# Optimization experiments

Hardware: AMD Instinct MI355X
Metric: run time of the kernel (lower is better)

## Reference

```python
import jax, jax.numpy as jnp
import numpy as np
import math

D = 1024
H = 16
DH = D // H
B, M, N = 4, 1024, 2048
LN_EPS = 1e-5


def setup_inputs() -> dict:
    key = jax.random.key(0)
    ks = jax.random.split(key, 8)
    s = 1.0 / math.sqrt(D)  # keep logits well-scaled
    return {
        "Q": jax.random.normal(ks[0], (B, M, D), jnp.float32),
        "KV": jax.random.normal(ks[1], (B, N, D), jnp.float32),
        "log_gate_bias": jax.random.normal(ks[2], (B, N), jnp.float32),
        "Wq": jax.random.normal(ks[3], (D, D), jnp.float32) * s,
        "bq": jnp.zeros((D,), jnp.float32),
        "Wk": jax.random.normal(ks[4], (D, D), jnp.float32) * s,
        "bk": jnp.zeros((D,), jnp.float32),
        "Wv": jax.random.normal(ks[5], (D, D), jnp.float32) * s,
        "bv": jnp.zeros((D,), jnp.float32),
        "Wo": jax.random.normal(ks[6], (D, D), jnp.float32) * s,
        "bo": jnp.zeros((D,), jnp.float32),
        "gamma": jnp.ones((D,), jnp.float32),
        "beta": jnp.zeros((D,), jnp.float32),
    }


def reference(Q, KV, log_gate_bias, Wq, bq, Wk, bk, Wv, bv, Wo, bo, gamma, beta):
    b, m, d = Q.shape
    n = KV.shape[1]
    # projections (torch Linear: x @ W.T + b), split heads -> (b, h, len, dh)
    q = (Q @ Wq.T + bq).reshape(b, m, H, DH).transpose(0, 2, 1, 3)
    k = (KV @ Wk.T + bk).reshape(b, n, H, DH).transpose(0, 2, 1, 3)
    v = (KV @ Wv.T + bv).reshape(b, n, H, DH).transpose(0, 2, 1, 3)
    scores = jnp.einsum('bhmd,bhnd->bhmn', q, k) / math.sqrt(DH)
    # additive gate bias broadcast over heads and queries: (b,1,1,n)
    scores = scores + log_gate_bias[:, None, None, :]
    attn = jax.nn.softmax(scores, axis=-1)
    out = jnp.einsum('bhmn,bhnd->bhmd', attn, v)
    out = out.transpose(0, 2, 1, 3).reshape(b, m, d)
    out = out @ Wo.T + bo
    # dropout p=0.0 (eval) -> identity; residual + LayerNorm
    x = Q + out
    mu = jnp.mean(x, axis=-1, keepdims=True)
    var = jnp.mean(jnp.square(x - mu), axis=-1, keepdims=True)
    return gamma * (x - mu) * jax.lax.rsqrt(var + LN_EPS) + beta
```

## Files before the change

kernel.cpp:

```cpp
#include <hip/hip_runtime.h>
#include <hip/hip_bf16.h>

#define DMODEL 1024
#define NHEAD  16
#define DHEAD  64
#define BB     4
#define MM     1024
#define NN     2048
#define LOG2E  1.4426950408889634f

typedef __attribute__((ext_vector_type(8))) short bf16x8;
typedef __attribute__((ext_vector_type(4))) float f32x4;

#define AS1 __attribute__((address_space(1)))
#define AS3 __attribute__((address_space(3)))

__device__ __forceinline__ unsigned short f2bf(float f) {
  unsigned int u = __builtin_bit_cast(unsigned int, f);
  unsigned int r = (u + 0x7fffu + ((u >> 16) & 1u)) >> 16;
  return (unsigned short)r;
}
__device__ __forceinline__ float bf2f(unsigned int u16) {
  return __builtin_bit_cast(float, u16 << 16);
}

__global__ __launch_bounds__(256)
void cast_all(const float* __restrict__ Q, const float* __restrict__ KV,
              const float* __restrict__ W0, const float* __restrict__ W1,
              const float* __restrict__ W2, const float* __restrict__ W3,
              unsigned short* __restrict__ oQ, unsigned short* __restrict__ oKV,
              unsigned short* __restrict__ o0, unsigned short* __restrict__ o1,
              unsigned short* __restrict__ o2, unsigned short* __restrict__ o3)
{
  const int bid = blockIdx.x;
  const float* s; unsigned short* d; int i;
  if (bid < 4096)       { s = Q;  d = oQ;  i = bid * 256 + threadIdx.x; }
  else if (bid < 12288) { s = KV; d = oKV; i = (bid - 4096) * 256 + threadIdx.x; }
  else {
    const int w = (bid - 12288) >> 10;
    s = w == 0 ? W0 : w == 1 ? W1 : w == 2 ? W2 : W3;
    d = w == 0 ? o0 : w == 1 ? o1 : w == 2 ? o2 : o3;
    i = ((bid - 12288) & 1023) * 256 + threadIdx.x;
  }
  const float4 v = ((const float4*)s)[i];
  union { unsigned short us[4]; unsigned long long u64; } o;
  o.us[0] = f2bf(v.x); o.us[1] = f2bf(v.y); o.us[2] = f2bf(v.z); o.us[3] = f2bf(v.w);
  *(unsigned long long*)(d + (size_t)i * 4) = o.u64;
}

__global__ __launch_bounds__(256)
void qkv_gemm(const unsigned short* __restrict__ Qbf,
              const unsigned short* __restrict__ KVbf,
              const unsigned short* __restrict__ Wqb,
              const unsigned short* __restrict__ Wkb,
              const unsigned short* __restrict__ Wvb,
              const float* __restrict__ bq, const float* __restrict__ bk,
              const float* __restrict__ bv,
              unsigned short* __restrict__ qout,
              unsigned short* __restrict__ kout,
              unsigned short* __restrict__ vtout)
{
  __shared__ unsigned short As[3][128 * 32];
  __shared__ unsigned short Ws[3][128 * 32];

  const int bid = blockIdx.x;
  const unsigned short* A; const unsigned short* W; const float* bias;
  int mode, lb, nmb;
  if (bid < 256)      { A = Qbf;  W = Wqb; bias = bq; mode = 0; lb = bid;       nmb = 4; }
  else if (bid < 768) { A = KVbf; W = Wkb; bias = bk; mode = 1; lb = bid - 256; nmb = 8; }
  else                { A = KVbf; W = Wvb; bias = bv; mode = 2; lb = bid - 768; nmb = 8; }
  const int xcd = lb & 7;
  const int l   = lb >> 3;
  const int mb  = xcd * nmb + (l >> 3);
  const int nb  = l & 7;

  const int tid  = threadIdx.x;
  const int wave = tid >> 6;
  const int lane = tid & 63;
  const int l15  = lane & 15;
  const int l4   = lane >> 4;
  const int wm   = wave >> 1;
  const int wn   = wave & 1;
  const size_t row0 = (size_t)mb * 128;
  const size_t col0 = (size_t)nb * 128;

  f32x4 acc[4][4] = {};

  const int cc0 = (wave * 2) * 64 + lane;
  const int cc1 = cc0 + 64;
  const int r0 = cc0 >> 2, sch0 = (cc0 & 3) ^ (r0 & 3);
  const int r1 = cc1 >> 2, sch1 = (cc1 & 3) ^ (r1 & 3);
  const unsigned short* ap0 = A + (row0 + r0) * DMODEL + sch0 * 8;
  const unsigned short* ap1 = A + (row0 + r1) * DMODEL + sch1 * 8;
  const unsigned short* wp0 = W + (col0 + r0) * DMODEL + sch0 * 8;
  const unsigned short* wp1 = W + (col0 + r1) * DMODEL + sch1 * 8;

  auto stage = [&](int buf) {
    __builtin_amdgcn_global_load_lds((const AS1 void*)ap0, (AS3 void*)(&As[buf][cc0 * 8]), 16, 0, 0);
    __builtin_amdgcn_global_load_lds((const AS1 void*)ap1, (AS3 void*)(&As[buf][cc1 * 8]), 16, 0, 0);
    __builtin_amdgcn_global_load_lds((const AS1 void*)wp0, (AS3 void*)(&Ws[buf][cc0 * 8]), 16, 0, 0);
    __builtin_amdgcn_global_load_lds((const AS1 void*)wp1, (AS3 void*)(&Ws[buf][cc1 * 8]), 16, 0, 0);
    ap0 += 32; ap1 += 32; wp0 += 32; wp1 += 32;
  };

  stage(0);
  stage(1);

  int cur = 0;
  for (int kt = 0; kt < 32; ++kt) {
    if (kt < 31) {
      asm volatile("s_waitcnt vmcnt(4)" ::: "memory");
    } else {
      asm volatile("s_waitcnt vmcnt(0)" ::: "memory");
    }
    __builtin_amdgcn_sched_barrier(0);
    __builtin_amdgcn_s_barrier();
    __builtin_amdgcn_sched_barrier(0);
    if (kt < 30) {
      int nxt = cur + 2; if (nxt >= 3) nxt -= 3;
      stage(nxt);
    }

    bf16x8 af[4], bfr[4];
#pragma unroll
    for (int mi = 0; mi < 4; ++mi) {
      int r = wm * 64 + mi * 16 + l15;
      af[mi] = *(const bf16x8*)&As[cur][r * 32 + ((l4 ^ (r & 3)) << 3)];
    }
#pragma unroll
    for (int ni = 0; ni < 4; ++ni) {
      int r = wn * 64 + ni * 16 + l15;
      bfr[ni] = *(const bf16x8*)&Ws[cur][r * 32 + ((l4 ^ (r & 3)) << 3)];
    }
    __builtin_amdgcn_s_setprio(1);
#pragma unroll
    for (int mi = 0; mi < 4; ++mi)
#pragma unroll
      for (int ni = 0; ni < 4; ++ni)
        acc[mi][ni] = __builtin_amdgcn_mfma_f32_16x16x32_bf16(af[mi], bfr[ni], acc[mi][ni], 0, 0, 0);
    __builtin_amdgcn_s_setprio(0);

    cur = (cur == 2) ? 0 : cur + 1;
  }

#pragma unroll
  for (int mi = 0; mi < 4; ++mi) {
#pragma unroll
    for (int ni = 0; ni < 4; ++ni) {
      const int col = (int)col0 + wn * 64 + ni * 16 + l15;
      const float bcol = bias[col];
      if (mode == 2) {
        const int row = (int)row0 + wm * 64 + mi * 16 + l4 * 4;
        const int b = row >> 11, n = row & 2047;
        const int h = col >> 6, d = col & 63;
        union { unsigned short us[4]; uint2 u; } pk;
#pragma unroll
        for (int i = 0; i < 4; ++i)
          pk.us[i] = __builtin_bit_cast(unsigned short, __float2bfloat16(acc[mi][ni][i] + bcol));
        *(uint2*)(vtout + (((size_t)(b * 16 + h) * 64 + d) << 11) + n) = pk.u;
      } else {
#pragma unroll
        for (int i = 0; i < 4; ++i) {
          const size_t row = row0 + wm * 64 + mi * 16 + l4 * 4 + i;
          float v = acc[mi][ni][i] + bcol;
          if (mode == 0) v *= (0.125f * LOG2E);
          (mode == 0 ? qout : kout)[row * DMODEL + col] =
            __builtin_bit_cast(unsigned short, __float2bfloat16(v));
        }
      }
    }
  }
}

__global__ __launch_bounds__(256)
void gemm_o(const unsigned short* __restrict__ A,
            const unsigned short* __restrict__ W,
            const float* __restrict__ bias,
            const unsigned short* __restrict__ resid,
            unsigned short* __restrict__ out)
{
  __shared__ unsigned short As[3][64 * 32];
  __shared__ unsigned short Ws[3][128 * 32];

  const int bid = blockIdx.x;
  const int xcd = bid & 7;
  const int l   = bid >> 3;
  const int mb  = xcd * 8 + (l >> 3);
  const int nb  = l & 7;

  const int tid  = threadIdx.x;
  const int wave = tid >> 6;
  const int lane = tid & 63;
  const int l15  = lane & 15;
  const int l4   = lane >> 4;
  const int wm   = wave >> 1;
  const int wn   = wave & 1;
  const size_t row0 = (size_t)mb * 64;
  const size_t col0 = (size_t)nb * 128;

  f32x4 acc[2][4] = {};

  const int ra = tid >> 2, scha = (tid & 3) ^ (ra & 3);
  const int cc0 = (wave * 2) * 64 + lane;
  const int cc1 = cc0 + 64;
  const int r0 = cc0 >> 2, sch0 = (cc0 & 3) ^ (r0 & 3);
  const int r1 = cc1 >> 2, sch1 = (cc1 & 3) ^ (r1 & 3);
  const unsigned short* ap  = A + (row0 + ra) * DMODEL + scha * 8;
  const unsigned short* wp0 = W + (col0 + r0) * DMODEL + sch0 * 8;
  const unsigned short* wp1 = W + (col0 + r1) * DMODEL + sch1 * 8;

  auto stage = [&](int buf) {
    __builtin_amdgcn_global_load_lds((const AS1 void*)ap,  (AS3 void*)(&As[buf][tid * 8]), 16, 0, 0);
    __builtin_amdgcn_global_load_lds((const AS1 void*)wp0, (AS3 void*)(&Ws[buf][cc0 * 8]), 16, 0, 0);
    __builtin_amdgcn_global_load_lds((const AS1 void*)wp1, (AS3 void*)(&Ws[buf][cc1 * 8]), 16, 0, 0);
    ap += 32; wp0 += 32; wp1 += 32;
  };

  stage(0);
  stage(1);

  int cur = 0;
  for (int kt = 0; kt < 32; ++kt) {
    if (kt < 31) {
      asm volatile("s_waitcnt vmcnt(3)" ::: "memory");
    } else {
      asm volatile("s_waitcnt vmcnt(0)" ::: "memory");
    }
    __builtin_amdgcn_sched_barrier(0);
    __builtin_amdgcn_s_barrier();
    __builtin_amdgcn_sched_barrier(0);
    if (kt < 30) {
      int nxt = cur + 2; if (nxt >= 3) nxt -= 3;
      stage(nxt);
    }

    bf16x8 af[2], bfr[4];
#pragma unroll
    for (int mi = 0; mi < 2; ++mi) {
      int r = wm * 32 + mi * 16 + l15;
      af[mi] = *(const bf16x8*)&As[cur][r * 32 + ((l4 ^ (r & 3)) << 3)];
    }
#pragma unroll
    for (int ni = 0; ni < 4; ++ni) {
      int r = wn * 64 + ni * 16 + l15;
      bfr[ni] = *(const bf16x8*)&Ws[cur][r * 32 + ((l4 ^ (r & 3)) << 3)];
    }
    __builtin_amdgcn_s_setprio(1);
#pragma unroll
    for (int mi = 0; mi < 2; ++mi)
#pragma unroll
      for (int ni = 0; ni < 4; ++ni)
        acc[mi][ni] = __builtin_amdgcn_mfma_f32_16x16x32_bf16(af[mi], bfr[ni], acc[mi][ni], 0, 0, 0);
    __builtin_amdgcn_s_setprio(0);

    cur = (cur == 2) ? 0 : cur + 1;
  }

#pragma unroll
  for (int mi = 0; mi < 2; ++mi) {
#pragma unroll
    for (int ni = 0; ni < 4; ++ni) {
      const int col = (int)col0 + wn * 64 + ni * 16 + l15;
      const float bcol = bias[col];
#pragma unroll
      for (int i = 0; i < 4; ++i) {
        const size_t row = row0 + wm * 32 + mi * 16 + l4 * 4 + i;
        const size_t idx = row * DMODEL + col;
        const float v = bf2f(resid[idx]) + acc[mi][ni][i] + bcol;
        out[idx] = __builtin_bit_cast(unsigned short, __float2bfloat16(v));
      }
    }
  }
}

__global__ __launch_bounds__(512, 4)
void attn_kernel(const unsigned short* __restrict__ qb,
                 const unsigned short* __restrict__ kb,
                 const unsigned short* __restrict__ vt,
                 const float* __restrict__ lgb,
                 unsigned short* __restrict__ attn)
{
  __shared__ unsigned short Ks[3][64 * 64];
  __shared__ unsigned short Vs[3][64 * 64];
  __shared__ float Gs[3][64];
  __shared__ unsigned short Ps[8][16 * 64];

  const int tid  = threadIdx.x;
  const int wave = tid >> 6;
  const int lane = tid & 63;
  const int l15  = lane & 15;
  const int l4   = lane >> 4;

  const int bid  = blockIdx.x;
  const int xcd  = bid & 7;
  const int slot = bid >> 3;
  const int m_i  = slot & 7;
  const int grp  = slot >> 3;
  const int bh   = grp * 8 + xcd;
  const int b    = bh >> 4;
  const int h    = bh & 15;
  const int m0   = m_i * 128;

  const unsigned short* qg = qb + ((size_t)(b * MM + m0)) * DMODEL + h * DHEAD;
  const unsigned short* kg = kb + ((size_t)b * NN) * DMODEL + h * DHEAD;
  const unsigned short* vg = vt + ((size_t)(b * NHEAD + h)) * (DHEAD * (size_t)NN);

  bf16x8 qf0, qf1;
  {
    const unsigned short* qrow = qg + (size_t)(wave * 16 + l15) * DMODEL;
    qf0 = *(const bf16x8*)(qrow + l4 * 8);
    qf1 = *(const bf16x8*)(qrow + 32 + l4 * 8);
  }

  bf16x8 ones;
  {
    const short one = (l15 == 0) ? (short)0x3f80 : (short)0;
#pragma unroll
    for (int j = 0; j < 8; ++j) ones[j] = one;
  }

  const int sr = tid >> 3;
  const int sc = (tid & 7) ^ (sr & 7);
  const unsigned short* kp = kg + (size_t)sr * DMODEL + (sc << 3);
  const unsigned short* vp = vg + (size_t)sr * NN + (sc << 3);
  const float* gp = lgb + (size_t)b * NN + lane;

  auto stage = [&](int buf) {
    if (wave == 0)
      __builtin_amdgcn_global_load_lds((const AS1 void*)gp, (AS3 void*)(&Gs[buf][lane]), 4, 0, 0);
    __builtin_amdgcn_global_load_lds((const AS1 void*)kp, (AS3 void*)(&Ks[buf][tid * 8]), 16, 0, 0);
    __builtin_amdgcn_global_load_lds((const AS1 void*)vp, (AS3 void*)(&Vs[buf][tid * 8]), 16, 0, 0);
    kp += 64 * DMODEL; vp += 64; gp += 64;
  };

  stage(0);
  stage(1);

  f32x4 ovec[5] = {};
  unsigned short* Pw = &Ps[wave][0];
  const int pbase = l15 * 128;
  const int s7 = l15 & 7;

  int cur = 0;
  for (int nt = 0; nt < NN / 64; ++nt) {
    if (nt < NN / 64 - 1) {
      if (wave == 0) asm volatile("s_waitcnt vmcnt(3)" ::: "memory");
      else           asm volatile("s_waitcnt vmcnt(2)" ::: "memory");
    } else {
      asm volatile("s_waitcnt vmcnt(0)" ::: "memory");
    }
    __builtin_amdgcn_sched_barrier(0);
    __builtin_amdgcn_s_barrier();
    __builtin_amdgcn_sched_barrier(0);
    if (nt < NN / 64 - 2) {
      int nxt = cur + 2; if (nxt >= 3) nxt -= 3;
      stage(nxt);
    }

    f32x4 s[4];
    __builtin_amdgcn_s_setprio(1);
#pragma unroll
    for (int ni = 0; ni < 4; ++ni) {
      const int r = ni * 16 + l15;
      const int c0 = l4 ^ (r & 7);
      bf16x8 kf0 = *(const bf16x8*)&Ks[cur][r * 64 + (c0 << 3)];
      bf16x8 kf1 = *(const bf16x8*)&Ks[cur][r * 64 + ((c0 ^ 4) << 3)];
      f32x4 z = {};
      z = __builtin_amdgcn_mfma_f32_16x16x32_bf16(kf0, qf0, z, 0, 0, 0);
      s[ni] = __builtin_amdgcn_mfma_f32_16x16x32_bf16(kf1, qf1, z, 0, 0, 0);
    }
    __builtin_amdgcn_s_setprio(0);

#pragma unroll
    for (int ni = 0; ni < 4; ++ni) {
      const float4 g = *(const float4*)&Gs[cur][ni * 16 + l4 * 4];
      union { unsigned short us[4]; uint2 u; } pk;
      pk.us[0] = __builtin_bit_cast(unsigned short,
                   __float2bfloat16(__builtin_amdgcn_exp2f(fmaf(g.x, LOG2E, s[ni][0]))));
      pk.us[1] = __builtin_bit_cast(unsigned short,
                   __float2bfloat16(__builtin_amdgcn_exp2f(fmaf(g.y, LOG2E, s[ni][1]))));
      pk.us[2] = __builtin_bit_cast(unsigned short,
                   __float2bfloat16(__builtin_amdgcn_exp2f(fmaf(g.z, LOG2E, s[ni][2]))));
      pk.us[3] = __builtin_bit_cast(unsigned short,
                   __float2bfloat16(__builtin_amdgcn_exp2f(fmaf(g.w, LOG2E, s[ni][3]))));
      *(uint2*)((char*)Pw + pbase + (((ni * 4 + l4) ^ (s7 << 1)) << 3)) = pk.u;
    }
    asm volatile("s_waitcnt lgkmcnt(0)" ::: "memory");
    __builtin_amdgcn_sched_barrier(0);

    __builtin_amdgcn_s_setprio(1);
#pragma unroll
    for (int ks2 = 0; ks2 < 2; ++ks2) {
      const bf16x8 pf = *(const bf16x8*)((const char*)Pw + pbase + (((ks2 * 4 + l4) ^ s7) << 4));
#pragma unroll
      for (int di = 0; di < 4; ++di) {
        const int d = di * 16 + l15;
        const bf16x8 vf = *(const bf16x8*)&Vs[cur][d * 64 + (((ks2 * 4 + l4) ^ (d & 7)) << 3)];
        ovec[di] = __builtin_amdgcn_mfma_f32_16x16x32_bf16(pf, vf, ovec[di], 0, 0, 0);
      }
      ovec[4] = __builtin_amdgcn_mfma_f32_16x16x32_bf16(pf, ones, ovec[4], 0, 0, 0);
    }
    __builtin_amdgcn_s_setprio(0);

    cur = (cur == 2) ? 0 : cur + 1;
  }

  const int lsrc = lane & 48;
  float linv[4];
#pragma unroll
  for (int i = 0; i < 4; ++i)
    linv[i] = 1.0f / __shfl(ovec[4][i], lsrc);
#pragma unroll
  for (int di = 0; di < 4; ++di)
#pragma unroll
    for (int i = 0; i < 4; ++i) {
      const int row = m0 + wave * 16 + l4 * 4 + i;
      const int col = h * DHEAD + di * 16 + l15;
      attn[((size_t)(b * MM + row)) * DMODEL + col] =
        __builtin_bit_cast(unsigned short, __float2bfloat16(ovec[di][i] * linv[i]));
    }
}

__global__ __launch_bounds__(256)
void ln_kernel(const unsigned short* __restrict__ x, const float* __restrict__ gamma,
               const float* __restrict__ beta, float* __restrict__ out)
{
  __shared__ float sh1[4], sh2[4];
  const int t = threadIdx.x;
  const size_t row = blockIdx.x;
  const uint2 raw = ((const uint2*)(x + row * DMODEL))[t];
  const float vx = bf2f(raw.x & 0xffffu);
  const float vy = bf2f(raw.x >> 16);
  const float vz = bf2f(raw.y & 0xffffu);
  const float vw = bf2f(raw.y >> 16);

  float s = vx + vy + vz + vw;
#pragma unroll
  for (int m = 1; m < 64; m <<= 1) s += __shfl_xor(s, m);
  if ((t & 63) == 0) sh1[t >> 6] = s;
  __syncthreads();
  const float mu = (sh1[0] + sh1[1] + sh1[2] + sh1[3]) * (1.0f / DMODEL);

  const float dx = vx - mu, dy = vy - mu, dz = vz - mu, dw = vw - mu;
  float q = dx * dx + dy * dy + dz * dz + dw * dw;
#pragma unroll
  for (int m = 1; m < 64; m <<= 1) q += __shfl_xor(q, m);
  if ((t & 63) == 0) sh2[t >> 6] = q;
  __syncthreads();
  const float var = (sh2[0] + sh2[1] + sh2[2] + sh2[3]) * (1.0f / DMODEL);
  const float rstd = rsqrtf(var + 1e-5f);

  const float4 g  = ((const float4*)gamma)[t];
  const float4 be = ((const float4*)beta)[t];
  float4 o;
  o.x = dx * rstd * g.x + be.x;
  o.y = dy * rstd * g.y + be.y;
  o.z = dz * rstd * g.z + be.z;
  o.w = dw * rstd * g.w + be.w;
  ((float4*)(out + row * DMODEL))[t] = o;
}

extern "C" void kernel_launch(void* const* d_in, const int* in_sizes, int n_in,
                              void* d_out, int out_size, void* d_ws, size_t ws_size,
                              hipStream_t stream)
{
  const float* Qf    = (const float*)d_in[0];
  const float* KVf   = (const float*)d_in[1];
  const float* lgb   = (const float*)d_in[2];
  const float* Wq    = (const float*)d_in[3];
  const float* bq    = (const float*)d_in[4];
  const float* Wk    = (const float*)d_in[5];
  const float* bk    = (const float*)d_in[6];
  const float* Wv    = (const float*)d_in[7];
  const float* bv    = (const float*)d_in[8];
  const float* Wo    = (const float*)d_in[9];
  const float* bo    = (const float*)d_in[10];
  const float* gamma = (const float*)d_in[11];
  const float* beta  = (const float*)d_in[12];
  float* out = (float*)d_out;

  char* ws = (char*)d_ws;
  unsigned short* Qbf   = (unsigned short*)(ws + 0);
  unsigned short* KVbf  = (unsigned short*)(ws + 8388608);
  unsigned short* attnb = (unsigned short*)(ws + 8388608);
  unsigned short* xbuf  = (unsigned short*)(ws + 16777216);
  unsigned short* Wqb = (unsigned short*)(ws + 25165824);
  unsigned short* Wkb = (unsigned short*)(ws + 27262976);
  unsigned short* Wvb = (unsigned short*)(ws + 29360128);
  unsigned short* Wob = (unsigned short*)(ws + 31457280);
  unsigned short* qbuf  = (unsigned short*)(ws + 33554432);
  unsigned short* kbuf  = (unsigned short*)(ws + 41943040);
  unsigned short* vtbuf = (unsigned short*)(ws + 58720256);

  cast_all<<<16384, dim3(256), 0, stream>>>(Qf, KVf, Wq, Wk, Wv, Wo,
                                            Qbf, KVbf, Wqb, Wkb, Wvb, Wob);

  qkv_gemm<<<1280, dim3(256), 0, stream>>>(Qbf, KVbf, Wqb, Wkb, Wvb,
                                           bq, bk, bv, qbuf, kbuf, vtbuf);

  attn_kernel<<<512, dim3(512), 0, stream>>>(qbuf, kbuf, vtbuf, lgb, attnb);

  gemm_o<<<512, dim3(256), 0, stream>>>(attnb, Wob, bo, Qbf, xbuf);

  ln_kernel<<<4096, dim3(256), 0, stream>>>(xbuf, gamma, beta, out);
}
```

Measured before the change: 152.5 us.

## Fuse K and V projections into one block sharing the KV tile

K and V projection blocks are merged so each block loads one KV activation tile and multiplies it against both Wk and Wv, keeping two accumulator sets. This halves the activation loads from global memory for the KV path and cuts the grid from 1280 to 768 blocks. The fused path uses double buffering instead of triple buffering, adds an extra barrier per iteration, and doubles the accumulator registers, which may reduce occupancy.

```diff
diff --git a/kernel.cpp b/kernel.cpp
--- a/kernel.cpp
+++ b/kernel.cpp
@@ -60,20 +60,9 @@
               unsigned short* __restrict__ kout,
               unsigned short* __restrict__ vtout)
 {
-  __shared__ unsigned short As[3][128 * 32];
-  __shared__ unsigned short Ws[3][128 * 32];
+  __shared__ unsigned short lds[24576];
 
   const int bid = blockIdx.x;
-  const unsigned short* A; const unsigned short* W; const float* bias;
-  int mode, lb, nmb;
-  if (bid < 256)      { A = Qbf;  W = Wqb; bias = bq; mode = 0; lb = bid;       nmb = 4; }
-  else if (bid < 768) { A = KVbf; W = Wkb; bias = bk; mode = 1; lb = bid - 256; nmb = 8; }
-  else                { A = KVbf; W = Wvb; bias = bv; mode = 2; lb = bid - 768; nmb = 8; }
-  const int xcd = lb & 7;
-  const int l   = lb >> 3;
-  const int mb  = xcd * nmb + (l >> 3);
-  const int nb  = l & 7;
-
   const int tid  = threadIdx.x;
   const int wave = tid >> 6;
   const int lane = tid & 63;
@@ -81,92 +70,202 @@
   const int l4   = lane >> 4;
   const int wm   = wave >> 1;
   const int wn   = wave & 1;
-  const size_t row0 = (size_t)mb * 128;
-  const size_t col0 = (size_t)nb * 128;
-
-  f32x4 acc[4][4] = {};
 
   const int cc0 = (wave * 2) * 64 + lane;
   const int cc1 = cc0 + 64;
   const int r0 = cc0 >> 2, sch0 = (cc0 & 3) ^ (r0 & 3);
   const int r1 = cc1 >> 2, sch1 = (cc1 & 3) ^ (r1 & 3);
-  const unsigned short* ap0 = A + (row0 + r0) * DMODEL + sch0 * 8;
-  const unsigned short* ap1 = A + (row0 + r1) * DMODEL + sch1 * 8;
-  const unsigned short* wp0 = W + (col0 + r0) * DMODEL + sch0 * 8;
-  const unsigned short* wp1 = W + (col0 + r1) * DMODEL + sch1 * 8;
-
-  auto stage = [&](int buf) {
-    __builtin_amdgcn_global_load_lds((const AS1 void*)ap0, (AS3 void*)(&As[buf][cc0 * 8]), 16, 0, 0);
-    __builtin_amdgcn_global_load_lds((const AS1 void*)ap1, (AS3 void*)(&As[buf][cc1 * 8]), 16, 0, 0);
-    __builtin_amdgcn_global_load_lds((const AS1 void*)wp0, (AS3 void*)(&Ws[buf][cc0 * 8]), 16, 0, 0);
-    __builtin_amdgcn_global_load_lds((const AS1 void*)wp1, (AS3 void*)(&Ws[buf][cc1 * 8]), 16, 0, 0);
-    ap0 += 32; ap1 += 32; wp0 += 32; wp1 += 32;
-  };
-
-  stage(0);
-  stage(1);
-
-  int cur = 0;
-  for (int kt = 0; kt < 32; ++kt) {
-    if (kt < 31) {
-      asm volatile("s_waitcnt vmcnt(4)" ::: "memory");
-    } else {
-      asm volatile("s_waitcnt vmcnt(0)" ::: "memory");
-    }
-    __builtin_amdgcn_sched_barrier(0);
-    __builtin_amdgcn_s_barrier();
-    __builtin_amdgcn_sched_barrier(0);
-    if (kt < 30) {
-      int nxt = cur + 2; if (nxt >= 3) nxt -= 3;
-      stage(nxt);
-    }
-
-    bf16x8 af[4], bfr[4];
+
+  if (bid < 256) {
+    const int xcd = bid & 7;
+    const int l   = bid >> 3;
+    const int mb  = xcd * 4 + (l >> 3);
+    const int nb  = l & 7;
+    const size_t row0 = (size_t)mb * 128;
+    const size_t col0 = (size_t)nb * 128;
+
+    unsigned short* As = lds;
+    unsigned short* Ws = lds + 12288;
+
+    f32x4 acc[4][4] = {};
+
+    const unsigned short* ap0 = Qbf + (row0 + r0) * DMODEL + sch0 * 8;
+    const unsigned short* ap1 = Qbf + (row0 + r1) * DMODEL + sch1 * 8;
+    const unsigned short* wp0 = Wqb + (col0 + r0) * DMODEL + sch0 * 8;
+    const unsigned short* wp1 = Wqb + (col0 + r1) * DMODEL + sch1 * 8;
+
+    auto stage = [&](int buf) {
+      __builtin_amdgcn_global_load_lds((const AS1 void*)ap0, (AS3 void*)(&As[buf * 4096 + cc0 * 8]), 16, 0, 0);
+      __builtin_amdgcn_global_load_lds((const AS1 void*)ap1, (AS3 void*)(&As[buf * 4096 + cc1 * 8]), 16, 0, 0);
+      __builtin_amdgcn_global_load_lds((const AS1 void*)wp0, (AS3 void*)(&Ws[buf * 4096 + cc0 * 8]), 16, 0, 0);
+      __builtin_amdgcn_global_load_lds((const AS1 void*)wp1, (AS3 void*)(&Ws[buf * 4096 + cc1 * 8]), 16, 0, 0);
+      ap0 += 32; ap1 += 32; wp0 += 32; wp1 += 32;
+    };
+
+    stage(0);
+    stage(1);
+
+    int cur = 0;
+    for (int kt = 0; kt < 32; ++kt) {
+      if (kt < 31) asm volatile("s_waitcnt vmcnt(4)" ::: "memory");
+      else         asm volatile("s_waitcnt vmcnt(0)" ::: "memory");
+      __builtin_amdgcn_sched_barrier(0);
+      __builtin_amdgcn_s_barrier();
+      __builtin_amdgcn_sched_barrier(0);
+      if (kt < 30) {
+        int nxt = cur + 2; if (nxt >= 3) nxt -= 3;
+        stage(nxt);
+      }
+
+      bf16x8 af[4], bfr[4];
+#pragma unroll
+      for (int mi = 0; mi < 4; ++mi) {
+        int r = wm * 64 + mi * 16 + l15;
+        af[mi] = *(const bf16x8*)&As[cur * 4096 + r * 32 + ((l4 ^ (r & 3)) << 3)];
+      }
+#pragma unroll
+      for (int ni = 0; ni < 4; ++ni) {
+        int r = wn * 64 + ni * 16 + l15;
+        bfr[ni] = *(const bf16x8*)&Ws[cur * 4096 + r * 32 + ((l4 ^ (r & 3)) << 3)];
+      }
+      __builtin_amdgcn_s_setprio(1);
+#pragma unroll
+      for (int mi = 0; mi < 4; ++mi)
+#pragma unroll
+        for (int ni = 0; ni < 4; ++ni)
+          acc[mi][ni] = __builtin_amdgcn_mfma_f32_16x16x32_bf16(af[mi], bfr[ni], acc[mi][ni], 0, 0, 0);
+      __builtin_amdgcn_s_setprio(0);
+
+      cur = (cur == 2) ? 0 : cur + 1;
+    }
+
 #pragma unroll
     for (int mi = 0; mi < 4; ++mi) {
-      int r = wm * 64 + mi * 16 + l15;
-      af[mi] = *(const bf16x8*)&As[cur][r * 32 + ((l4 ^ (r & 3)) << 3)];
-    }
-#pragma unroll
-    for (int ni = 0; ni < 4; ++ni) {
-      int r = wn * 64 + ni * 16 + l15;
-      bfr[ni] = *(const bf16x8*)&Ws[cur][r * 32 + ((l4 ^ (r & 3)) << 3)];
-    }
-    __builtin_amdgcn_s_setprio(1);
-#pragma unroll
-    for (int mi = 0; mi < 4; ++mi)
-#pragma unroll
-      for (int ni = 0; ni < 4; ++ni)
-        acc[mi][ni] = __builtin_amdgcn_mfma_f32_16x16x32_bf16(af[mi], bfr[ni], acc[mi][ni], 0, 0, 0);
-    __builtin_amdgcn_s_setprio(0);
-
-    cur = (cur == 2) ? 0 : cur + 1;
-  }
-
-#pragma unroll
-  for (int mi = 0; mi < 4; ++mi) {
-#pragma unroll
-    for (int ni = 0; ni < 4; ++ni) {
-      const int col = (int)col0 + wn * 64 + ni * 16 + l15;
-      const float bcol = bias[col];
-      if (mode == 2) {
+#pragma unroll
+      for (int ni = 0; ni < 4; ++ni) {
+        const int col = (int)col0 + wn * 64 + ni * 16 + l15;
+        const float bcol = bq[col];
+#pragma unroll
+        for (int i = 0; i < 4; ++i) {
+          const size_t row = row0 + wm * 64 + mi * 16 + l4 * 4 + i;
+          const float v = (acc[mi][ni][i] + bcol) * (0.125f * LOG2E);
+          qout[row * DMODEL + col] = __builtin_bit_cast(unsigned short, __float2bfloat16(v));
+        }
+      }
+    }
+  } else {
+    const int lb2 = bid - 256;
+    const int xcd = lb2 & 7;
+    const int l   = lb2 >> 3;
+    const int mb  = xcd * 8 + (l >> 3);
+    const int nb  = l & 7;
+    const size_t row0 = (size_t)mb * 128;
+    const size_t col0 = (size_t)nb * 128;
+
+    unsigned short* A2  = lds;
+    unsigned short* Wk2 = lds + 8192;
+    unsigned short* Wv2 = lds + 16384;
+
+    f32x4 acck[4][4] = {};
+    f32x4 accv[4][4] = {};
+
+    const unsigned short* ap0  = KVbf + (row0 + r0) * DMODEL + sch0 * 8;
+    const unsigned short* ap1  = KVbf + (row0 + r1) * DMODEL + sch1 * 8;
+    const unsigned short* wkp0 = Wkb + (col0 + r0) * DMODEL + sch0 * 8;
+    const unsigned short* wkp1 = Wkb + (col0 + r1) * DMODEL + sch1 * 8;
+    const unsigned short* wvp0 = Wvb + (col0 + r0) * DMODEL + sch0 * 8;
+    const unsigned short* wvp1 = Wvb + (col0 + r1) * DMODEL + sch1 * 8;
+
+    auto stage = [&](int buf) {
+      __builtin_amdgcn_global_load_lds((const AS1 void*)ap0,  (AS3 void*)(&A2 [buf * 4096 + cc0 * 8]), 16, 0, 0);
+      __builtin_amdgcn_global_load_lds((const AS1 void*)ap1,  (AS3 void*)(&A2 [buf * 4096 + cc1 * 8]), 16, 0, 0);
+      __builtin_amdgcn_global_load_lds((const AS1 void*)wkp0, (AS3 void*)(&Wk2[buf * 4096 + cc0 * 8]), 16, 0, 0);
+      __builtin_amdgcn_global_load_lds((const AS1 void*)wkp1, (AS3 void*)(&Wk2[buf * 4096 + cc1 * 8]), 16, 0, 0);
+      __builtin_amdgcn_global_load_lds((const AS1 void*)wvp0, (AS3 void*)(&Wv2[buf * 4096 + cc0 * 8]), 16, 0, 0);
+      __builtin_amdgcn_global_load_lds((const AS1 void*)wvp1, (AS3 void*)(&Wv2[buf * 4096 + cc1 * 8]), 16, 0, 0);
+      ap0 += 32; ap1 += 32; wkp0 += 32; wkp1 += 32; wvp0 += 32; wvp1 += 32;
+    };
+
+    stage(0);
+
+    for (int kt = 0; kt < 32; ++kt) {
+      const int cur = kt & 1;
+      if (kt < 31) {
+        stage(cur ^ 1);
+        asm volatile("s_waitcnt vmcnt(6)" ::: "memory");
+      } else {
+        asm volatile("s_waitcnt vmcnt(0)" ::: "memory");
+      }
+      __builtin_amdgcn_sched_barrier(0);
+      __builtin_amdgcn_s_barrier();
+      __builtin_amdgcn_sched_barrier(0);
+
+      bf16x8 af[4], fr[4];
+#pragma unroll
+      for (int mi = 0; mi < 4; ++mi) {
+        int r = wm * 64 + mi * 16 + l15;
+        af[mi] = *(const bf16x8*)&A2[cur * 4096 + r * 32 + ((l4 ^ (r & 3)) << 3)];
+      }
+#pragma unroll
+      for (int ni = 0; ni < 4; ++ni) {
+        int r = wn * 64 + ni * 16 + l15;
+        fr[ni] = *(const bf16x8*)&Wk2[cur * 4096 + r * 32 + ((l4 ^ (r & 3)) << 3)];
+      }
+      __builtin_amdgcn_s_setprio(1);
+#pragma unroll
+      for (int mi = 0; mi < 4; ++mi)
+#pragma unroll
+        for (int ni = 0; ni < 4; ++ni)
+          acck[mi][ni] = __builtin_amdgcn_mfma_f32_16x16x32_bf16(af[mi], fr[ni], acck[mi][ni], 0, 0, 0);
+      __builtin_amdgcn_s_setprio(0);
+
+#pragma unroll
+      for (int ni = 0; ni < 4; ++ni) {
+        int r = wn * 64 + ni * 16 + l15;
+        fr[ni] = *(const bf16x8*)&Wv2[cur * 4096 + r * 32 + ((l4 ^ (r & 3)) << 3)];
+      }
+      __builtin_amdgcn_s_setprio(1);
+#pragma unroll
+      for (int mi = 0; mi < 4; ++mi)
+#pragma unroll
+        for (int ni = 0; ni < 4; ++ni)
+          accv[mi][ni] = __builtin_amdgcn_mfma_f32_16x16x32_bf16(af[mi], fr[ni], accv[mi][ni], 0, 0, 0);
+      __builtin_amdgcn_s_setprio(0);
+
+      asm volatile("s_waitcnt lgkmcnt(0)" ::: "memory");
+      __builtin_amdgcn_sched_barrier(0);
+      __builtin_amdgcn_s_barrier();
+      __builtin_amdgcn_sched_barrier(0);
+    }
+
+#pragma unroll
+    for (int mi = 0; mi < 4; ++mi) {
+#pragma unroll
+      for (int ni = 0; ni < 4; ++ni) {
+        const int col = (int)col0 + wn * 64 + ni * 16 + l15;
+        const float bcol = bk[col];
+#pragma unroll
+        for (int i = 0; i < 4; ++i) {
+          const size_t row = row0 + wm * 64 + mi * 16 + l4 * 4 + i;
+          kout[row * DMODEL + col] = __builtin_bit_cast(unsigned short,
+              __float2bfloat16(acck[mi][ni][i] + bcol));
+        }
+      }
+    }
+#pragma unroll
+    for (int mi = 0; mi < 4; ++mi) {
+#pragma unroll
+      for (int ni = 0; ni < 4; ++ni) {
+        const int col = (int)col0 + wn * 64 + ni * 16 + l15;
+        const float bcol = bv[col];
         const int row = (int)row0 + wm * 64 + mi * 16 + l4 * 4;
         const int b = row >> 11, n = row & 2047;
         const int h = col >> 6, d = col & 63;
         union { unsigned short us[4]; uint2 u; } pk;
 #pragma unroll
         for (int i = 0; i < 4; ++i)
-          pk.us[i] = __builtin_bit_cast(unsigned short, __float2bfloat16(acc[mi][ni][i] + bcol));
+          pk.us[i] = __builtin_bit_cast(unsigned short, __float2bfloat16(accv[mi][ni][i] + bcol));
         *(uint2*)(vtout + (((size_t)(b * 16 + h) * 64 + d) << 11) + n) = pk.u;
-      } else {
-#pragma unroll
-        for (int i = 0; i < 4; ++i) {
-          const size_t row = row0 + wm * 64 + mi * 16 + l4 * 4 + i;
-          float v = acc[mi][ni][i] + bcol;
-          if (mode == 0) v *= (0.125f * LOG2E);
-          (mode == 0 ? qout : kout)[row * DMODEL + col] =
-            __builtin_bit_cast(unsigned short, __float2bfloat16(v));
-        }
       }
     }
   }
@@ -495,8 +594,8 @@
   cast_all<<<16384, dim3(256), 0, stream>>>(Qf, KVf, Wq, Wk, Wv, Wo,
                                             Qbf, KVbf, Wqb, Wkb, Wvb, Wob);
 
-  qkv_gemm<<<1280, dim3(256), 0, stream>>>(Qbf, KVbf, Wqb, Wkb, Wvb,
-                                           bq, bk, bv, qbuf, kbuf, vtbuf);
+  qkv_gemm<<<768, dim3(256), 0, stream>>>(Qbf, KVbf, Wqb, Wkb, Wvb,
+                                          bq, bk, bv, qbuf, kbuf, vtbuf);
 
   attn_kernel<<<512, dim3(512), 0, stream>>>(qbuf, kbuf, vtbuf, lgb, attnb);
 
```

Result: slower. 166.3 us (+9.0%).
